# Kernel optimization log

Measured on AMD Instinct MI355X. Metric: run time of the kernel, lower is better.

Reference implementation:

```python
import jax, jax.numpy as jnp
import numpy as np

N_NODES = 100000
N_EDGES = 1600000
D = 128
K = 3
LAMBDA_MAX = 2.0  # PyG ChebConv default for normalization='sym'


def _cheb_conv(x, row, col, w, diag, lins, bias):
    # x: [N, D]; w: [E] scaled-Laplacian off-diag weights; diag: scalar diag weight
    # lins: [K, D, D]; bias: [D]
    n = x.shape[0]

    def prop(v):
        # out[col] += w * v[row]  (sparse L_hat @ v), plus diagonal term
        return jax.ops.segment_sum(w[:, None] * v[row], col, num_segments=n) + diag * v

    Tx0 = x
    out = Tx0 @ lins[0]
    Tx1 = prop(Tx0)
    out = out + Tx1 @ lins[1]
    for k in range(2, lins.shape[0]):
        Tx2 = 2.0 * prop(Tx1) - Tx0
        out = out + Tx2 @ lins[k]
        Tx0, Tx1 = Tx1, Tx2
    return out + bias


def setup_inputs() -> dict:
    key = jax.random.key(0)
    ks = jax.random.split(key, 10)
    glorot = float(np.sqrt(6.0 / (D + D)))
    X = jax.random.normal(ks[0], (N_NODES, D), dtype=jnp.float32)
    edge_index = jax.random.randint(ks[1], (2, N_EDGES), 0, N_NODES, dtype=jnp.int64)
    edge_weight = jax.random.uniform(ks[2], (N_EDGES,), dtype=jnp.float32)
    H = jax.random.normal(ks[3], (N_NODES, D), dtype=jnp.float32)
    C = jax.random.normal(ks[4], (N_NODES, D), dtype=jnp.float32)
    # gate order: i, f, c, o
    W = jax.random.uniform(ks[5], (4, D, D), dtype=jnp.float32, minval=-glorot, maxval=glorot)
    b = jnp.zeros((4, D), dtype=jnp.float32)
    conv_W = jax.random.uniform(ks[6], (4, K, D, D), dtype=jnp.float32, minval=-glorot, maxval=glorot)
    conv_b = jnp.zeros((4, D), dtype=jnp.float32)
    return {"X": X, "edge_index": edge_index, "edge_weight": edge_weight,
            "H": H, "C": C, "W": W, "b": b, "conv_W": conv_W, "conv_b": conv_b}


def reference(X, edge_index, edge_weight, H, C, W, b, conv_W, conv_b):
    n = X.shape[0]
    row, col = edge_index[0], edge_index[1]
    # sym-normalized Laplacian, scaled: L_hat = 2L/lmax - I
    deg = jax.ops.segment_sum(edge_weight, row, num_segments=n)
    dinv = jnp.where(deg > 0, deg ** -0.5, 0.0)
    w = -(dinv[row] * edge_weight * dinv[col]) * (2.0 / LAMBDA_MAX)
    diag = 2.0 / LAMBDA_MAX - 1.0  # scalar (0.0 when lmax == 2)

    def gate(g):
        return X @ W[g] + _cheb_conv(H, row, col, w, diag, conv_W[g], conv_b[g]) + b[g]

    I = jax.nn.sigmoid(gate(0))
    F = jax.nn.sigmoid(gate(1))
    T = jnp.tanh(gate(2))
    C_new = F * C + I * T
    O = jax.nn.sigmoid(gate(3))
    H_new = O * jnp.tanh(C_new)
    return H_new
```

## Files before the change

### kernel.cpp

```cpp
#include <hip/hip_runtime.h>

#define N_NODES 100000
#define N_EDGES 1600000
#define CAP 64

typedef unsigned short ushort_t;
typedef __attribute__((ext_vector_type(8))) short bf16x8;
typedef __attribute__((ext_vector_type(4))) float f32x4;
typedef __attribute__((ext_vector_type(4))) int int4e;
typedef __attribute__((ext_vector_type(4))) unsigned short ushort4e;

__device__ __forceinline__ unsigned short f2bf(float f) {
  unsigned int u = __float_as_uint(f);
  u = (u + 0x7FFFu + ((u >> 16) & 1u)) >> 16;
  return (unsigned short)u;
}

__global__ __launch_bounds__(256) void k_misc(
    const int* __restrict__ ei, const float* __restrict__ ew,
    const float* __restrict__ X, const float* __restrict__ H,
    float* __restrict__ deg, ushort_t* __restrict__ U,
    const float* __restrict__ W, const float* __restrict__ b,
    const float* __restrict__ cW, const float* __restrict__ cb,
    ushort_t* __restrict__ Bt, float* __restrict__ bias) {
  int bid = blockIdx.x;
  if (bid < 6250) {
    int e = bid * 256 + threadIdx.x;
    atomicAdd(&deg[ei[e]], ew[e]);
  } else if (bid < 18750) {
    int i = (bid - 6250) * 256 + threadIdx.x;
    int n = i >> 5, q = i & 31;
    float4 x = *(const float4*)(X + (size_t)n * 128 + q * 4);
    float4 h = *(const float4*)(H + (size_t)n * 128 + q * 4);
    ushort4 a, bb;
    a.x = f2bf(x.x); a.y = f2bf(x.y); a.z = f2bf(x.z); a.w = f2bf(x.w);
    bb.x = f2bf(h.x); bb.y = f2bf(h.y); bb.z = f2bf(h.z); bb.w = f2bf(h.w);
    *(ushort4*)(U + (size_t)n * 512 + q * 4) = a;
    *(ushort4*)(U + (size_t)n * 512 + 128 + q * 4) = bb;
  } else {
    int idx = (bid - 18750) * 256 + threadIdx.x;
    int j = idx >> 9, k = idx & 511;
    int dd = j >> 2, g = j & 3;
    float v;
    if (k < 128) v = W[(g * 128 + k) * 128 + dd];
    else {
      int kk = k - 128;
      int blk = kk >> 7;
      v = cW[((g * 3 + blk) * 128 + (kk & 127)) * 128 + dd];
    }
    Bt[idx] = f2bf(v);
    if (k == 0) bias[j] = b[g * 128 + dd] + cb[g * 128 + dd];
  }
}

__global__ void k_bucket(const int* __restrict__ ei, const float* __restrict__ ew,
                         const float* __restrict__ deg, int* __restrict__ cnt,
                         int2* __restrict__ bE) {
  int e = blockIdx.x * 256 + threadIdx.x;
  if (e >= N_EDGES) return;
  int r = ei[e], c = ei[N_EDGES + e];
  float dr = deg[r];
  float s = dr > 0.f ? rsqrtf(dr) * ew[e] : 0.f;
  int pos = atomicAdd(&cnt[c], 1);
  if (pos < CAP) bE[c * CAP + pos] = make_int2(r, __float_as_int(s));
}

#define FMA4(A, W, V) \
  A.x = fmaf(W, V.x, A.x); A.y = fmaf(W, V.y, A.y); \
  A.z = fmaf(W, V.z, A.z); A.w = fmaf(W, V.w, A.w);

#define GATH(vv, p) { \
  ushort4 rw = *(const ushort4*)(sb + (size_t)(p) * 512); \
  vv.x = __uint_as_float((unsigned)rw.x << 16); \
  vv.y = __uint_as_float((unsigned)rw.y << 16); \
  vv.z = __uint_as_float((unsigned)rw.z << 16); \
  vv.w = __uint_as_float((unsigned)rw.w << 16); }

template <int PHASE>
__global__ __launch_bounds__(256) void k_gather(
    const int* __restrict__ cnt, const int2* __restrict__ bE,
    const float* __restrict__ deg, const float* __restrict__ H,
    ushort_t* __restrict__ U) {
  int g = threadIdx.x >> 5, lane = threadIdx.x & 31;
  int node = blockIdx.x * 8 + g;
  if (node >= N_NODES) return;
  int cn = cnt[node]; if (cn > CAP) cn = CAP;
  const int2* be = bE + node * CAP;
  const ushort_t* sb = U + (PHASE == 1 ? 128 : 256) + lane * 4;
  float dc = deg[node];
  float sc = dc > 0.f ? -rsqrtf(dc) : 0.f;

  float4 z = {0.f, 0.f, 0.f, 0.f};
  float4 a0 = z, a1 = z, a2 = z, a3 = z, a4 = z, a5 = z, a6 = z, a7 = z;
  int i = 0;
  for (; i + 8 <= cn; i += 8) {
    int4e p0 = __builtin_nontemporal_load((const int4e*)(be + i));
    int4e p1 = __builtin_nontemporal_load((const int4e*)(be + i + 2));
    int4e p2 = __builtin_nontemporal_load((const int4e*)(be + i + 4));
    int4e p3 = __builtin_nontemporal_load((const int4e*)(be + i + 6));
    float4 v0, v1, v2, v3, v4, v5, v6, v7;
    GATH(v0, p0.x); GATH(v1, p0.z); GATH(v2, p1.x); GATH(v3, p1.z);
    GATH(v4, p2.x); GATH(v5, p2.z); GATH(v6, p3.x); GATH(v7, p3.z);
    FMA4(a0, __int_as_float(p0.y), v0); FMA4(a1, __int_as_float(p0.w), v1);
    FMA4(a2, __int_as_float(p1.y), v2); FMA4(a3, __int_as_float(p1.w), v3);
    FMA4(a4, __int_as_float(p2.y), v4); FMA4(a5, __int_as_float(p2.w), v5);
    FMA4(a6, __int_as_float(p3.y), v6); FMA4(a7, __int_as_float(p3.w), v7);
  }
  for (; i + 4 <= cn; i += 4) {
    int4e p0 = __builtin_nontemporal_load((const int4e*)(be + i));
    int4e p1 = __builtin_nontemporal_load((const int4e*)(be + i + 2));
    float4 v0, v1, v2, v3;
    GATH(v0, p0.x); GATH(v1, p0.z); GATH(v2, p1.x); GATH(v3, p1.z);
    FMA4(a0, __int_as_float(p0.y), v0); FMA4(a1, __int_as_float(p0.w), v1);
    FMA4(a2, __int_as_float(p1.y), v2); FMA4(a3, __int_as_float(p1.w), v3);
  }
  for (; i < cn; ++i) {
    int2 p = be[i];
    float4 v;
    GATH(v, p.x);
    FMA4(a0, __int_as_float(p.y), v);
  }
  float4 acc;
  acc.x = sc * (((a0.x + a1.x) + (a2.x + a3.x)) + ((a4.x + a5.x) + (a6.x + a7.x)));
  acc.y = sc * (((a0.y + a1.y) + (a2.y + a3.y)) + ((a4.y + a5.y) + (a6.y + a7.y)));
  acc.z = sc * (((a0.z + a1.z) + (a2.z + a3.z)) + ((a4.z + a5.z) + (a6.z + a7.z)));
  acc.w = sc * (((a0.w + a1.w) + (a2.w + a3.w)) + ((a4.w + a5.w) + (a6.w + a7.w)));

  if (PHASE == 1) {
    ushort4e u = {f2bf(acc.x), f2bf(acc.y), f2bf(acc.z), f2bf(acc.w)};
    __builtin_nontemporal_store(u, (ushort4e*)(U + (size_t)node * 512 + 256 + lane * 4));
  } else {
    float4 h = *(const float4*)(H + (size_t)node * 128 + lane * 4);
    ushort4e u = {f2bf(2.f * acc.x - h.x), f2bf(2.f * acc.y - h.y),
                  f2bf(2.f * acc.z - h.z), f2bf(2.f * acc.w - h.w)};
    __builtin_nontemporal_store(u, (ushort4e*)(U + (size_t)node * 512 + 384 + lane * 4));
  }
}

__global__ __launch_bounds__(256) void k_gemm(
    const ushort_t* __restrict__ U, const ushort_t* __restrict__ Bt,
    const float* __restrict__ bias, const float* __restrict__ C,
    float* __restrict__ out) {
  __shared__ char ldsRaw[65536];
  char* ldsA0 = ldsRaw;
  char* ldsB0 = ldsRaw + 16384;
  char* ldsA1 = ldsRaw + 32768;
  char* ldsB1 = ldsRaw + 49152;
  float* ldsF = (float*)ldsRaw;

  const int tid = threadIdx.x;
  const int lane = tid & 63;
  const int w = tid >> 6;
  const int wr = w >> 1, wc = w & 1;
  const int b = blockIdx.x;
  const int g = (b & 7) * 391 + (b >> 3);
  const int m0 = (g >> 2) * 128;
  const int n0 = (g & 3) * 128;
  const int l15 = lane & 15;
  const int l4 = lane >> 4;

  auto stage_half = [&](int kt, char* la_base, char* lb_base, int h) {
    const int k0 = kt * 64;
#pragma unroll
    for (int is = 2 * h; is < 2 * h + 2; ++is) {
      int s = is * 256 + tid;
      int row = s >> 3;
      int cs = (s & 7) ^ (row & 7);
      const ushort_t* ga = U + (size_t)(m0 + row) * 512 + k0 + cs * 8;
      const ushort_t* gb = Bt + (size_t)(n0 + row) * 512 + k0 + cs * 8;
      char* la = la_base + (is * 256 + (tid & 192)) * 16;
      char* lb = lb_base + (is * 256 + (tid & 192)) * 16;
      __builtin_amdgcn_global_load_lds((const __attribute__((address_space(1))) void*)ga,
                                       (__attribute__((address_space(3))) void*)la, 16, 0, 0);
      __builtin_amdgcn_global_load_lds((const __attribute__((address_space(1))) void*)gb,
                                       (__attribute__((address_space(3))) void*)lb, 16, 0, 0);
    }
  };

  const int fcol = tid & 31;
  const int rbase = tid >> 5;
  float cpre[16];
#pragma unroll
  for (int half = 0; half < 2; ++half)
#pragma unroll
    for (int k = 0; k < 8; ++k) {
      int n = m0 + half * 64 + rbase + k * 8;
      int dg = (n0 >> 2) + fcol;
      cpre[half * 8 + k] = (n < N_NODES) ? C[(size_t)n * 128 + dg] : 0.f;
    }

  int offA[2][4], offB[2][4];
#pragma unroll
  for (int ks = 0; ks < 2; ++ks) {
    int slot = ((ks * 4 + l4) ^ (l15 & 7)) * 16;
#pragma unroll
    for (int i = 0; i < 4; ++i) {
      offA[ks][i] = (wr * 64 + i * 16 + l15) * 128 + slot;
      offB[ks][i] = (wc * 64 + i * 16 + l15) * 128 + slot;
    }
  }

  f32x4 acc[4][4] = {};

  stage_half(0, ldsA0, ldsB0, 0);
  stage_half(0, ldsA0, ldsB0, 1);

  for (int kt = 0; kt < 8; ++kt) {
    char* curA = (kt & 1) ? ldsA1 : ldsA0;
    char* curB = (kt & 1) ? ldsB1 : ldsB0;
    char* nA = (kt & 1) ? ldsA0 : ldsA1;
    char* nB = (kt & 1) ? ldsB0 : ldsB1;
    if (kt < 7) {
      stage_half(kt + 1, nA, nB, 0);
      asm volatile("s_waitcnt vmcnt(4)" ::: "memory");
    } else {
      asm volatile("s_waitcnt vmcnt(0)" ::: "memory");
    }
    __builtin_amdgcn_s_barrier();
    __builtin_amdgcn_sched_barrier(0);

    {
      bf16x8 af[4], bfr[4];
#pragma unroll
      for (int mi = 0; mi < 4; ++mi) af[mi] = *(const bf16x8*)(curA + offA[0][mi]);
#pragma unroll
      for (int ni = 0; ni < 4; ++ni) bfr[ni] = *(const bf16x8*)(curB + offB[0][ni]);
      asm volatile("s_waitcnt lgkmcnt(0)" ::: "memory");
      __builtin_amdgcn_sched_barrier(0);
      __builtin_amdgcn_s_setprio(1);
#pragma unroll
      for (int mi = 0; mi < 4; ++mi)
#pragma unroll
        for (int ni = 0; ni < 4; ++ni)
          acc[mi][ni] = __builtin_amdgcn_mfma_f32_16x16x32_bf16(af[mi], bfr[ni], acc[mi][ni], 0, 0, 0);
      __builtin_amdgcn_s_setprio(0);
    }
    if (kt < 7) stage_half(kt + 1, nA, nB, 1);
    {
      bf16x8 af[4], bfr[4];
#pragma unroll
      for (int mi = 0; mi < 4; ++mi) af[mi] = *(const bf16x8*)(curA + offA[1][mi]);
#pragma unroll
      for (int ni = 0; ni < 4; ++ni) bfr[ni] = *(const bf16x8*)(curB + offB[1][ni]);
      asm volatile("s_waitcnt lgkmcnt(0)" ::: "memory");
      __builtin_amdgcn_sched_barrier(0);
      __builtin_amdgcn_s_setprio(1);
#pragma unroll
      for (int mi = 0; mi < 4; ++mi)
#pragma unroll
        for (int ni = 0; ni < 4; ++ni)
          acc[mi][ni] = __builtin_amdgcn_mfma_f32_16x16x32_bf16(af[mi], bfr[ni], acc[mi][ni], 0, 0, 0);
      __builtin_amdgcn_s_setprio(0);
    }
    __builtin_amdgcn_s_barrier();
  }

#pragma unroll
  for (int half = 0; half < 2; ++half) {
    if (wr == half) {
#pragma unroll
      for (int ni = 0; ni < 4; ++ni) {
        int col = wc * 64 + ni * 16 + l15;
        float bv = bias[n0 + col];
#pragma unroll
        for (int mi = 0; mi < 4; ++mi)
#pragma unroll
          for (int r = 0; r < 4; ++r)
            ldsF[(mi * 16 + l4 * 4 + r) * 132 + col] = acc[mi][ni][r] + bv;
      }
    }
    __syncthreads();
#pragma unroll
    for (int k = 0; k < 8; ++k) {
      int p = tid + k * 256;
      int rl = p >> 5, f = p & 31;
      int n = m0 + half * 64 + rl;
      if (n < N_NODES) {
        float4 pre = *(const float4*)&ldsF[rl * 132 + f * 4];
        int dg = (n0 >> 2) + f;
        float ig = __builtin_amdgcn_rcpf(1.f + __expf(-pre.x));
        float fg = __builtin_amdgcn_rcpf(1.f + __expf(-pre.y));
        float ec = __expf(-2.f * fabsf(pre.z));
        float tg = __builtin_copysignf((1.f - ec) * __builtin_amdgcn_rcpf(1.f + ec), pre.z);
        float og = __builtin_amdgcn_rcpf(1.f + __expf(-pre.w));
        float cOld = cpre[half * 8 + k];
        float cn = fg * cOld + ig * tg;
        float en = __expf(-2.f * fabsf(cn));
        float th = __builtin_copysignf((1.f - en) * __builtin_amdgcn_rcpf(1.f + en), cn);
        out[(size_t)n * 128 + dg] = og * th;
      }
    }
    __syncthreads();
  }
}

extern "C" void kernel_launch(void* const* d_in, const int* in_sizes, int n_in,
                              void* d_out, int out_size, void* d_ws, size_t ws_size,
                              hipStream_t stream) {
  const float* X  = (const float*)d_in[0];
  const int*   ei = (const int*)d_in[1];
  const float* ew = (const float*)d_in[2];
  const float* H  = (const float*)d_in[3];
  const float* C  = (const float*)d_in[4];
  const float* W  = (const float*)d_in[5];
  const float* b  = (const float*)d_in[6];
  const float* cW = (const float*)d_in[7];
  const float* cb = (const float*)d_in[8];
  float* out = (float*)d_out;
  char* ws = (char*)d_ws;

  float*    deg  = (float*)(ws);
  int*      cnt  = (int*)(ws + 0x80000);
  int2*     bE   = (int2*)(ws + 0x100000);
  ushort_t* U    = (ushort_t*)(ws + 0x3500000);
  ushort_t* Bt   = (ushort_t*)(ws + 0x9700000);
  float*    bias = (float*)(ws + 0x9780000);

  hipMemsetAsync(ws, 0, 0x100000, stream);

  k_misc<<<19774, 256, 0, stream>>>(ei, ew, X, H, deg, U, W, b, cW, cb, Bt, bias);
  k_bucket<<<(N_EDGES + 255) / 256, 256, 0, stream>>>(ei, ew, deg, cnt, bE);
  k_gather<1><<<(N_NODES + 7) / 8, 256, 0, stream>>>(cnt, bE, deg, H, U);
  k_gather<2><<<(N_NODES + 7) / 8, 256, 0, stream>>>(cnt, bE, deg, H, U);
  k_gemm<<<3128, 256, 0, stream>>>(U, Bt, bias, C, out);
}
```

Before: 464.8 us.

## Merge edge bucketing into misc kernel and apply source degree scaling in gather

Result: slower. 501.6 us (+7.9%).

```diff
diff --git a/kernel.cpp b/kernel.cpp
--- a/kernel.cpp
+++ b/kernel.cpp
@@ -19,50 +19,51 @@
 __global__ __launch_bounds__(256) void k_misc(
     const int* __restrict__ ei, const float* __restrict__ ew,
     const float* __restrict__ X, const float* __restrict__ H,
-    float* __restrict__ deg, ushort_t* __restrict__ U,
+    float* __restrict__ deg, int* __restrict__ cnt, int2* __restrict__ bE,
+    ushort_t* __restrict__ U,
     const float* __restrict__ W, const float* __restrict__ b,
     const float* __restrict__ cW, const float* __restrict__ cb,
     ushort_t* __restrict__ Bt, float* __restrict__ bias) {
   int bid = blockIdx.x;
-  if (bid < 6250) {
-    int e = bid * 256 + threadIdx.x;
-    atomicAdd(&deg[ei[e]], ew[e]);
-  } else if (bid < 18750) {
-    int i = (bid - 6250) * 256 + threadIdx.x;
-    int n = i >> 5, q = i & 31;
-    float4 x = *(const float4*)(X + (size_t)n * 128 + q * 4);
-    float4 h = *(const float4*)(H + (size_t)n * 128 + q * 4);
-    ushort4 a, bb;
-    a.x = f2bf(x.x); a.y = f2bf(x.y); a.z = f2bf(x.z); a.w = f2bf(x.w);
-    bb.x = f2bf(h.x); bb.y = f2bf(h.y); bb.z = f2bf(h.z); bb.w = f2bf(h.w);
-    *(ushort4*)(U + (size_t)n * 512 + q * 4) = a;
-    *(ushort4*)(U + (size_t)n * 512 + 128 + q * 4) = bb;
+  int role = bid & 7, q = bid >> 3;
+  if (role < 2) {
+    int e = (q * 2 + role) * 256 + threadIdx.x;
+    if (e < N_EDGES) atomicAdd(&deg[ei[e]], ew[e]);
+  } else if (role < 4) {
+    int e = (q * 2 + (role - 2)) * 256 + threadIdx.x;
+    if (e < N_EDGES) {
+      int r = ei[e], c = ei[N_EDGES + e];
+      float w = ew[e];
+      int pos = atomicAdd(&cnt[c], 1);
+      if (pos < CAP) bE[c * CAP + pos] = make_int2(r, __float_as_int(w));
+    }
   } else {
-    int idx = (bid - 18750) * 256 + threadIdx.x;
-    int j = idx >> 9, k = idx & 511;
-    int dd = j >> 2, g = j & 3;
-    float v;
-    if (k < 128) v = W[(g * 128 + k) * 128 + dd];
-    else {
-      int kk = k - 128;
-      int blk = kk >> 7;
-      v = cW[((g * 3 + blk) * 128 + (kk & 127)) * 128 + dd];
-    }
-    Bt[idx] = f2bf(v);
-    if (k == 0) bias[j] = b[g * 128 + dd] + cb[g * 128 + dd];
-  }
-}
-
-__global__ void k_bucket(const int* __restrict__ ei, const float* __restrict__ ew,
-                         const float* __restrict__ deg, int* __restrict__ cnt,
-                         int2* __restrict__ bE) {
-  int e = blockIdx.x * 256 + threadIdx.x;
-  if (e >= N_EDGES) return;
-  int r = ei[e], c = ei[N_EDGES + e];
-  float dr = deg[r];
-  float s = dr > 0.f ? rsqrtf(dr) * ew[e] : 0.f;
-  int pos = atomicAdd(&cnt[c], 1);
-  if (pos < CAP) bE[c * CAP + pos] = make_int2(r, __float_as_int(s));
+    int s = q * 4 + (role - 4);
+    if (s < 12500) {
+      int i = s * 256 + threadIdx.x;
+      int n = i >> 5, qq = i & 31;
+      float4 x = *(const float4*)(X + (size_t)n * 128 + qq * 4);
+      float4 h = *(const float4*)(H + (size_t)n * 128 + qq * 4);
+      ushort4 a, bb;
+      a.x = f2bf(x.x); a.y = f2bf(x.y); a.z = f2bf(x.z); a.w = f2bf(x.w);
+      bb.x = f2bf(h.x); bb.y = f2bf(h.y); bb.z = f2bf(h.z); bb.w = f2bf(h.w);
+      *(ushort4*)(U + (size_t)n * 512 + qq * 4) = a;
+      *(ushort4*)(U + (size_t)n * 512 + 128 + qq * 4) = bb;
+    } else if (s < 13524) {
+      int idx = (s - 12500) * 256 + threadIdx.x;
+      int j = idx >> 9, k = idx & 511;
+      int dd = j >> 2, g = j & 3;
+      float v;
+      if (k < 128) v = W[(g * 128 + k) * 128 + dd];
+      else {
+        int kk = k - 128;
+        int blk = kk >> 7;
+        v = cW[((g * 3 + blk) * 128 + (kk & 127)) * 128 + dd];
+      }
+      Bt[idx] = f2bf(v);
+      if (k == 0) bias[j] = b[g * 128 + dd] + cb[g * 128 + dd];
+    }
+  }
 }
 
 #define FMA4(A, W, V) \
@@ -75,6 +76,8 @@
   vv.y = __uint_as_float((unsigned)rw.y << 16); \
   vv.z = __uint_as_float((unsigned)rw.z << 16); \
   vv.w = __uint_as_float((unsigned)rw.w << 16); }
+
+#define EDGW(dd, wbits) ((dd) > 0.f ? rsqrtf(dd) * __int_as_float(wbits) : 0.f)
 
 template <int PHASE>
 __global__ __launch_bounds__(256) void k_gather(
@@ -98,27 +101,31 @@
     int4e p1 = __builtin_nontemporal_load((const int4e*)(be + i + 2));
     int4e p2 = __builtin_nontemporal_load((const int4e*)(be + i + 4));
     int4e p3 = __builtin_nontemporal_load((const int4e*)(be + i + 6));
+    float d0 = deg[p0.x], d1 = deg[p0.z], d2 = deg[p1.x], d3 = deg[p1.z];
+    float d4 = deg[p2.x], d5 = deg[p2.z], d6 = deg[p3.x], d7 = deg[p3.z];
     float4 v0, v1, v2, v3, v4, v5, v6, v7;
     GATH(v0, p0.x); GATH(v1, p0.z); GATH(v2, p1.x); GATH(v3, p1.z);
     GATH(v4, p2.x); GATH(v5, p2.z); GATH(v6, p3.x); GATH(v7, p3.z);
-    FMA4(a0, __int_as_float(p0.y), v0); FMA4(a1, __int_as_float(p0.w), v1);
-    FMA4(a2, __int_as_float(p1.y), v2); FMA4(a3, __int_as_float(p1.w), v3);
-    FMA4(a4, __int_as_float(p2.y), v4); FMA4(a5, __int_as_float(p2.w), v5);
-    FMA4(a6, __int_as_float(p3.y), v6); FMA4(a7, __int_as_float(p3.w), v7);
+    FMA4(a0, EDGW(d0, p0.y), v0); FMA4(a1, EDGW(d1, p0.w), v1);
+    FMA4(a2, EDGW(d2, p1.y), v2); FMA4(a3, EDGW(d3, p1.w), v3);
+    FMA4(a4, EDGW(d4, p2.y), v4); FMA4(a5, EDGW(d5, p2.w), v5);
+    FMA4(a6, EDGW(d6, p3.y), v6); FMA4(a7, EDGW(d7, p3.w), v7);
   }
   for (; i + 4 <= cn; i += 4) {
     int4e p0 = __builtin_nontemporal_load((const int4e*)(be + i));
     int4e p1 = __builtin_nontemporal_load((const int4e*)(be + i + 2));
+    float d0 = deg[p0.x], d1 = deg[p0.z], d2 = deg[p1.x], d3 = deg[p1.z];
     float4 v0, v1, v2, v3;
     GATH(v0, p0.x); GATH(v1, p0.z); GATH(v2, p1.x); GATH(v3, p1.z);
-    FMA4(a0, __int_as_float(p0.y), v0); FMA4(a1, __int_as_float(p0.w), v1);
-    FMA4(a2, __int_as_float(p1.y), v2); FMA4(a3, __int_as_float(p1.w), v3);
+    FMA4(a0, EDGW(d0, p0.y), v0); FMA4(a1, EDGW(d1, p0.w), v1);
+    FMA4(a2, EDGW(d2, p1.y), v2); FMA4(a3, EDGW(d3, p1.w), v3);
   }
   for (; i < cn; ++i) {
     int2 p = be[i];
+    float dd = deg[p.x];
     float4 v;
     GATH(v, p.x);
-    FMA4(a0, __int_as_float(p.y), v);
+    FMA4(a0, EDGW(dd, p.y), v);
   }
   float4 acc;
   acc.x = sc * (((a0.x + a1.x) + (a2.x + a3.x)) + ((a4.x + a5.x) + (a6.x + a7.x)));
@@ -318,8 +325,7 @@
 
   hipMemsetAsync(ws, 0, 0x100000, stream);
 
-  k_misc<<<19774, 256, 0, stream>>>(ei, ew, X, H, deg, U, W, b, cW, cb, Bt, bias);
-  k_bucket<<<(N_EDGES + 255) / 256, 256, 0, stream>>>(ei, ew, deg, cnt, bE);
+  k_misc<<<27128, 256, 0, stream>>>(ei, ew, X, H, deg, cnt, bE, U, W, b, cW, cb, Bt, bias);
   k_gather<1><<<(N_NODES + 7) / 8, 256, 0, stream>>>(cnt, bE, deg, H, U);
   k_gather<2><<<(N_NODES + 7) / 8, 256, 0, stream>>>(cnt, bE, deg, H, U);
   k_gemm<<<3128, 256, 0, stream>>>(U, Bt, bias, C, out);
```

## Load GEMM B fragments directly from global and halve LDS for occupancy

Applied to the files above, without the earlier changes.

Result: slower. 526.5 us (+13.3%).

```diff
diff --git a/kernel.cpp b/kernel.cpp
--- a/kernel.cpp
+++ b/kernel.cpp
@@ -137,15 +137,13 @@
   }
 }
 
-__global__ __launch_bounds__(256) void k_gemm(
+__global__ __launch_bounds__(256, 4) void k_gemm(
     const ushort_t* __restrict__ U, const ushort_t* __restrict__ Bt,
     const float* __restrict__ bias, const float* __restrict__ C,
     float* __restrict__ out) {
-  __shared__ char ldsRaw[65536];
+  __shared__ char ldsRaw[33792];
   char* ldsA0 = ldsRaw;
-  char* ldsB0 = ldsRaw + 16384;
-  char* ldsA1 = ldsRaw + 32768;
-  char* ldsB1 = ldsRaw + 49152;
+  char* ldsA1 = ldsRaw + 16384;
   float* ldsF = (float*)ldsRaw;
 
   const int tid = threadIdx.x;
@@ -159,99 +157,80 @@
   const int l15 = lane & 15;
   const int l4 = lane >> 4;
 
-  auto stage_half = [&](int kt, char* la_base, char* lb_base, int h) {
+  auto stageA = [&](int kt, char* la_base) {
     const int k0 = kt * 64;
 #pragma unroll
-    for (int is = 2 * h; is < 2 * h + 2; ++is) {
+    for (int is = 0; is < 4; ++is) {
       int s = is * 256 + tid;
       int row = s >> 3;
       int cs = (s & 7) ^ (row & 7);
       const ushort_t* ga = U + (size_t)(m0 + row) * 512 + k0 + cs * 8;
-      const ushort_t* gb = Bt + (size_t)(n0 + row) * 512 + k0 + cs * 8;
       char* la = la_base + (is * 256 + (tid & 192)) * 16;
-      char* lb = lb_base + (is * 256 + (tid & 192)) * 16;
       __builtin_amdgcn_global_load_lds((const __attribute__((address_space(1))) void*)ga,
                                        (__attribute__((address_space(3))) void*)la, 16, 0, 0);
-      __builtin_amdgcn_global_load_lds((const __attribute__((address_space(1))) void*)gb,
-                                       (__attribute__((address_space(3))) void*)lb, 16, 0, 0);
     }
   };
 
-  const int fcol = tid & 31;
-  const int rbase = tid >> 5;
-  float cpre[16];
-#pragma unroll
-  for (int half = 0; half < 2; ++half)
-#pragma unroll
-    for (int k = 0; k < 8; ++k) {
-      int n = m0 + half * 64 + rbase + k * 8;
-      int dg = (n0 >> 2) + fcol;
-      cpre[half * 8 + k] = (n < N_NODES) ? C[(size_t)n * 128 + dg] : 0.f;
-    }
-
-  int offA[2][4], offB[2][4];
+  int offA[2][4];
 #pragma unroll
   for (int ks = 0; ks < 2; ++ks) {
     int slot = ((ks * 4 + l4) ^ (l15 & 7)) * 16;
 #pragma unroll
-    for (int i = 0; i < 4; ++i) {
+    for (int i = 0; i < 4; ++i)
       offA[ks][i] = (wr * 64 + i * 16 + l15) * 128 + slot;
-      offB[ks][i] = (wc * 64 + i * 16 + l15) * 128 + slot;
-    }
-  }
+  }
+  const ushort_t* Bb = Bt + (size_t)(n0 + wc * 64 + l15) * 512 + l4 * 8;
 
   f32x4 acc[4][4] = {};
 
-  stage_half(0, ldsA0, ldsB0, 0);
-  stage_half(0, ldsA0, ldsB0, 1);
+  stageA(0, ldsA0);
 
   for (int kt = 0; kt < 8; ++kt) {
-    char* curA = (kt & 1) ? ldsA1 : ldsA0;
-    char* curB = (kt & 1) ? ldsB1 : ldsB0;
-    char* nA = (kt & 1) ? ldsA0 : ldsA1;
-    char* nB = (kt & 1) ? ldsB0 : ldsB1;
+    char* cur = (kt & 1) ? ldsA1 : ldsA0;
+    char* nxt = (kt & 1) ? ldsA0 : ldsA1;
+    bf16x8 b0[4], b1[4];
+#pragma unroll
+    for (int ni = 0; ni < 4; ++ni)
+      b0[ni] = *(const bf16x8*)(Bb + ni * 16 * 512 + kt * 64);
+#pragma unroll
+    for (int ni = 0; ni < 4; ++ni)
+      b1[ni] = *(const bf16x8*)(Bb + ni * 16 * 512 + kt * 64 + 32);
+    __builtin_amdgcn_sched_barrier(0);
     if (kt < 7) {
-      stage_half(kt + 1, nA, nB, 0);
-      asm volatile("s_waitcnt vmcnt(4)" ::: "memory");
+      stageA(kt + 1, nxt);
+      __builtin_amdgcn_sched_barrier(0);
+      asm volatile("s_waitcnt vmcnt(12)" ::: "memory");
     } else {
-      asm volatile("s_waitcnt vmcnt(0)" ::: "memory");
+      asm volatile("s_waitcnt vmcnt(8)" ::: "memory");
     }
     __builtin_amdgcn_s_barrier();
     __builtin_amdgcn_sched_barrier(0);
-
     {
-      bf16x8 af[4], bfr[4];
-#pragma unroll
-      for (int mi = 0; mi < 4; ++mi) af[mi] = *(const bf16x8*)(curA + offA[0][mi]);
-#pragma unroll
-      for (int ni = 0; ni < 4; ++ni) bfr[ni] = *(const bf16x8*)(curB + offB[0][ni]);
-      asm volatile("s_waitcnt lgkmcnt(0)" ::: "memory");
-      __builtin_amdgcn_sched_barrier(0);
+      bf16x8 af[4];
+#pragma unroll
+      for (int mi = 0; mi < 4; ++mi) af[mi] = *(const bf16x8*)(cur + offA[0][mi]);
       __builtin_amdgcn_s_setprio(1);
 #pragma unroll
       for (int mi = 0; mi < 4; ++mi)
 #pragma unroll
         for (int ni = 0; ni < 4; ++ni)
-          acc[mi][ni] = __builtin_amdgcn_mfma_f32_16x16x32_bf16(af[mi], bfr[ni], acc[mi][ni], 0, 0, 0);
+          acc[mi][ni] = __builtin_amdgcn_mfma_f32_16x16x32_bf16(af[mi], b0[ni], acc[mi][ni], 0, 0, 0);
       __builtin_amdgcn_s_setprio(0);
     }
-    if (kt < 7) stage_half(kt + 1, nA, nB, 1);
     {
-      bf16x8 af[4], bfr[4];
-#pragma unroll
-      for (int mi = 0; mi < 4; ++mi) af[mi] = *(const bf16x8*)(curA + offA[1][mi]);
-#pragma unroll
-      for (int ni = 0; ni < 4; ++ni) bfr[ni] = *(const bf16x8*)(curB + offB[1][ni]);
-      asm volatile("s_waitcnt lgkmcnt(0)" ::: "memory");
-      __builtin_amdgcn_sched_barrier(0);
+      bf16x8 af[4];
+#pragma unroll
+      for (int mi = 0; mi < 4; ++mi) af[mi] = *(const bf16x8*)(cur + offA[1][mi]);
       __builtin_amdgcn_s_setprio(1);
 #pragma unroll
       for (int mi = 0; mi < 4; ++mi)
 #pragma unroll
         for (int ni = 0; ni < 4; ++ni)
-          acc[mi][ni] = __builtin_amdgcn_mfma_f32_16x16x32_bf16(af[mi], bfr[ni], acc[mi][ni], 0, 0, 0);
+          acc[mi][ni] = __builtin_amdgcn_mfma_f32_16x16x32_bf16(af[mi], b1[ni], acc[mi][ni], 0, 0, 0);
       __builtin_amdgcn_s_setprio(0);
     }
+    asm volatile("s_waitcnt lgkmcnt(0)" ::: "memory");
+    __builtin_amdgcn_sched_barrier(0);
     __builtin_amdgcn_s_barrier();
   }
 
@@ -283,7 +262,7 @@
         float ec = __expf(-2.f * fabsf(pre.z));
         float tg = __builtin_copysignf((1.f - ec) * __builtin_amdgcn_rcpf(1.f + ec), pre.z);
         float og = __builtin_amdgcn_rcpf(1.f + __expf(-pre.w));
-        float cOld = cpre[half * 8 + k];
+        float cOld = C[(size_t)n * 128 + dg];
         float cn = fg * cOld + ig * tg;
         float en = __expf(-2.f * fabsf(cn));
         float th = __builtin_copysignf((1.f - en) * __builtin_amdgcn_rcpf(1.f + en), cn);
```
